# Optimization experiments

Hardware: AMD Instinct MI355X
Metric: run time of the kernel (lower is better)

## Reference

```python
import jax, jax.numpy as jnp
import numpy as np

B = 1_000_000
FEAT = 64
EMBEDDING_SIZE = 128


def setup_inputs() -> dict:
    key = jax.random.key(0)
    k0, k1, k2 = jax.random.split(key, 3)
    x = jax.random.normal(k0, (B, FEAT), dtype=jnp.float32)
    W1 = jax.random.normal(k1, (FEAT, FEAT), dtype=jnp.float32) * (1.0 / np.sqrt(FEAT))
    b1 = jnp.zeros((FEAT,), dtype=jnp.float32)
    W2 = jax.random.normal(k2, (FEAT, EMBEDDING_SIZE), dtype=jnp.float32) * (1.0 / np.sqrt(FEAT))
    b2 = jnp.zeros((EMBEDDING_SIZE,), dtype=jnp.float32)
    return {"x": x, "W1": W1, "b1": b1, "W2": W2, "b2": b2}


def reference(x, W1, b1, W2, b2):
    # head: Linear(64,64) -> ReLU -> Linear(64, EMBEDDING_SIZE)
    h = jax.nn.relu(x @ W1 + b1)
    e = h @ W2 + b2
    # per-sample L2 normalize with zero-norm guard (Normalize module)
    norm = jnp.linalg.norm(e, axis=-1, keepdims=True)  # [B,1]
    out = jnp.where(norm == 0, jnp.zeros_like(e), e / jnp.where(norm == 0, 1.0, norm))
    return out
```

## Files before the change

### kernel.cpp

```cpp
#include <hip/hip_runtime.h>
#include <stdint.h>


typedef __attribute__((ext_vector_type(8))) short short8;
typedef __attribute__((ext_vector_type(4))) float f32x4;

__device__ __forceinline__ ushort f2bf(float f) {
    union { float f; uint32_t u; } v; v.f = f;
    uint32_t u = v.u;
    u += 0x7fffu + ((u >> 16) & 1u);
    return (ushort)(u >> 16);
}

__global__ __launch_bounds__(256)
void fused_head_kernel(const float* __restrict__ x,
                       const float* __restrict__ W1,
                       const float* __restrict__ b1,
                       const float* __restrict__ W2,
                       const float* __restrict__ b2,
                       float* __restrict__ out,
                       int ntiles)
{
    __shared__ ushort w1t[64][72];
    __shared__ ushort w2t[128][72];
    __shared__ ushort htile[4][16][72];

    const int tid  = threadIdx.x;
    const int wave = tid >> 6;
    const int lane = tid & 63;
    const int l16  = lane & 15;
    const int lq   = lane >> 4;

    for (int idx = tid; idx < 64 * 64; idx += 256) {
        int k = idx >> 6, n = idx & 63;
        w1t[n][k] = f2bf(W1[idx]);
    }
    for (int idx = tid; idx < 64 * 128; idx += 256) {
        int k = idx >> 7, n = idx & 127;
        w2t[n][k] = f2bf(W2[idx]);
    }
    float b1v[4], b2v[8];
#pragma unroll
    for (int nt = 0; nt < 4; ++nt) b1v[nt] = b1[l16 + 16 * nt];
#pragma unroll
    for (int nt = 0; nt < 8; ++nt) b2v[nt] = b2[l16 + 16 * nt];
    __syncthreads();

    for (int tile = blockIdx.x; tile < ntiles; tile += gridDim.x) {
        const int r0 = tile * 64 + wave * 16;

        short8 xf[2];
#pragma unroll
        for (int t = 0; t < 2; ++t) {
            const float* p = x + (size_t)(r0 + l16) * 64 + t * 32 + lq * 8;
            f32x4 u0 = *(const f32x4*)p;
            f32x4 u1 = *(const f32x4*)(p + 4);
            short8 v;
            v[0] = (short)f2bf(u0[0]); v[1] = (short)f2bf(u0[1]);
            v[2] = (short)f2bf(u0[2]); v[3] = (short)f2bf(u0[3]);
            v[4] = (short)f2bf(u1[0]); v[5] = (short)f2bf(u1[1]);
            v[6] = (short)f2bf(u1[2]); v[7] = (short)f2bf(u1[3]);
            xf[t] = v;
        }

        f32x4 acc1[4] = {};
#pragma unroll
        for (int t = 0; t < 2; ++t) {
#pragma unroll
            for (int nt = 0; nt < 4; ++nt) {
                short8 bf = *(const short8*)&w1t[l16 + 16 * nt][t * 32 + lq * 8];
                acc1[nt] = __builtin_amdgcn_mfma_f32_16x16x32_bf16(xf[t], bf, acc1[nt], 0, 0, 0);
            }
        }
#pragma unroll
        for (int nt = 0; nt < 4; ++nt) {
#pragma unroll
            for (int r = 0; r < 4; ++r) {
                float h = acc1[nt][r] + b1v[nt];
                h = h > 0.f ? h : 0.f;
                htile[wave][lq * 4 + r][l16 + 16 * nt] = f2bf(h);
            }
        }

        f32x4 acc2[8] = {};
#pragma unroll
        for (int t = 0; t < 2; ++t) {
            short8 af = *(const short8*)&htile[wave][l16][t * 32 + lq * 8];
#pragma unroll
            for (int nt = 0; nt < 8; ++nt) {
                short8 bf = *(const short8*)&w2t[l16 + 16 * nt][t * 32 + lq * 8];
                acc2[nt] = __builtin_amdgcn_mfma_f32_16x16x32_bf16(af, bf, acc2[nt], 0, 0, 0);
            }
        }

        float ss[4] = {0.f, 0.f, 0.f, 0.f};
#pragma unroll
        for (int nt = 0; nt < 8; ++nt) {
#pragma unroll
            for (int r = 0; r < 4; ++r) {
                float e = acc2[nt][r] + b2v[nt];
                acc2[nt][r] = e;
                ss[r] += e * e;
            }
        }
#pragma unroll
        for (int m = 1; m < 16; m <<= 1) {
#pragma unroll
            for (int r = 0; r < 4; ++r) ss[r] += __shfl_xor(ss[r], m, 64);
        }

#pragma unroll
        for (int r = 0; r < 4; ++r) {
            float s = ss[r];
            float sc = s > 0.f ? rsqrtf(s) : 0.f;
            float* po = out + (size_t)(r0 + lq * 4 + r) * 128 + l16;
#pragma unroll
            for (int nt = 0; nt < 8; ++nt) po[nt * 16] = acc2[nt][r] * sc;
        }
    }
}

extern "C" void kernel_launch(void* const* d_in, const int* in_sizes, int n_in,
                              void* d_out, int out_size, void* d_ws, size_t ws_size,
                              hipStream_t stream) {
    const float* x  = (const float*)d_in[0];
    const float* W1 = (const float*)d_in[1];
    const float* b1 = (const float*)d_in[2];
    const float* W2 = (const float*)d_in[3];
    const float* b2 = (const float*)d_in[4];
    float* out = (float*)d_out;

    const int nrows  = in_sizes[0] / 64;
    const int ntiles = nrows / 64;
    int grid = ntiles < 3125 ? ntiles : 3125;

    hipLaunchKernelGGL(fused_head_kernel, dim3(grid), dim3(256), 0, stream,
                       x, W1, b1, W2, b2, out, ntiles);
}
```

Baseline: 676.5 us.

## Software-pipeline x loads, transpose MFMA operands for vectorized row-major stores

Double-buffers the per-tile x loads in registers, so the next tile's global reads are issued before the current tile is computed. The MFMA operand order is swapped so each lane holds four contiguous output columns of a single row. That allows 16-byte vector stores and a two-step shuffle reduction for the norm in place of a four-step one. Biases move to shared memory, read as float4, and launch bounds request 4 blocks per CU, which raises register pressure from the two prefetch buffers.

```diff
diff --git a/kernel.cpp b/kernel.cpp
--- a/kernel.cpp
+++ b/kernel.cpp
@@ -11,8 +11,11 @@
     u += 0x7fffu + ((u >> 16) & 1u);
     return (ushort)(u >> 16);
 }
+__device__ __forceinline__ uint32_t pack2(float a, float b) {
+    return (uint32_t)f2bf(a) | ((uint32_t)f2bf(b) << 16);
+}
 
-__global__ __launch_bounds__(256)
+__global__ __launch_bounds__(256, 4)
 void fused_head_kernel(const float* __restrict__ x,
                        const float* __restrict__ W1,
                        const float* __restrict__ b1,
@@ -24,12 +27,23 @@
     __shared__ ushort w1t[64][72];
     __shared__ ushort w2t[128][72];
     __shared__ ushort htile[4][16][72];
+    __shared__ __align__(16) float b1s[64];
+    __shared__ __align__(16) float b2s[128];
 
     const int tid  = threadIdx.x;
     const int wave = tid >> 6;
     const int lane = tid & 63;
     const int l16  = lane & 15;
     const int lq   = lane >> 4;
+
+    int tile = blockIdx.x;
+
+    f32x4 uA[4], uB[4];
+    {
+        const float* p = x + ((size_t)(tile * 64 + wave * 16 + l16)) * 64 + lq * 8;
+        uA[0] = *(const f32x4*)p;        uA[1] = *(const f32x4*)(p + 4);
+        uA[2] = *(const f32x4*)(p + 32); uA[3] = *(const f32x4*)(p + 36);
+    }
 
     for (int idx = tid; idx < 64 * 64; idx += 256) {
         int k = idx >> 6, n = idx & 63;
@@ -39,84 +53,97 @@
         int k = idx >> 7, n = idx & 127;
         w2t[n][k] = f2bf(W2[idx]);
     }
-    float b1v[4], b2v[8];
-#pragma unroll
-    for (int nt = 0; nt < 4; ++nt) b1v[nt] = b1[l16 + 16 * nt];
-#pragma unroll
-    for (int nt = 0; nt < 8; ++nt) b2v[nt] = b2[l16 + 16 * nt];
+    if (tid < 64)  b1s[tid] = b1[tid];
+    if (tid < 128) b2s[tid] = b2[tid];
     __syncthreads();
 
-    for (int tile = blockIdx.x; tile < ntiles; tile += gridDim.x) {
-        const int r0 = tile * 64 + wave * 16;
+    auto loadx = [&](f32x4* u, int t) {
+        const float* p = x + ((size_t)(t * 64 + wave * 16 + l16)) * 64 + lq * 8;
+        u[0] = *(const f32x4*)p;        u[1] = *(const f32x4*)(p + 4);
+        u[2] = *(const f32x4*)(p + 32); u[3] = *(const f32x4*)(p + 36);
+    };
 
+    auto process = [&](const f32x4* u, int t) {
         short8 xf[2];
 #pragma unroll
-        for (int t = 0; t < 2; ++t) {
-            const float* p = x + (size_t)(r0 + l16) * 64 + t * 32 + lq * 8;
-            f32x4 u0 = *(const f32x4*)p;
-            f32x4 u1 = *(const f32x4*)(p + 4);
+        for (int h = 0; h < 2; ++h) {
             short8 v;
-            v[0] = (short)f2bf(u0[0]); v[1] = (short)f2bf(u0[1]);
-            v[2] = (short)f2bf(u0[2]); v[3] = (short)f2bf(u0[3]);
-            v[4] = (short)f2bf(u1[0]); v[5] = (short)f2bf(u1[1]);
-            v[6] = (short)f2bf(u1[2]); v[7] = (short)f2bf(u1[3]);
-            xf[t] = v;
+            v[0] = (short)f2bf(u[2*h][0]);   v[1] = (short)f2bf(u[2*h][1]);
+            v[2] = (short)f2bf(u[2*h][2]);   v[3] = (short)f2bf(u[2*h][3]);
+            v[4] = (short)f2bf(u[2*h+1][0]); v[5] = (short)f2bf(u[2*h+1][1]);
+            v[6] = (short)f2bf(u[2*h+1][2]); v[7] = (short)f2bf(u[2*h+1][3]);
+            xf[h] = v;
         }
 
         f32x4 acc1[4] = {};
 #pragma unroll
-        for (int t = 0; t < 2; ++t) {
+        for (int h = 0; h < 2; ++h)
 #pragma unroll
             for (int nt = 0; nt < 4; ++nt) {
-                short8 bf = *(const short8*)&w1t[l16 + 16 * nt][t * 32 + lq * 8];
-                acc1[nt] = __builtin_amdgcn_mfma_f32_16x16x32_bf16(xf[t], bf, acc1[nt], 0, 0, 0);
+                short8 wf = *(const short8*)&w1t[nt * 16 + l16][h * 32 + lq * 8];
+                acc1[nt] = __builtin_amdgcn_mfma_f32_16x16x32_bf16(wf, xf[h], acc1[nt], 0, 0, 0);
             }
-        }
+
 #pragma unroll
         for (int nt = 0; nt < 4; ++nt) {
-#pragma unroll
-            for (int r = 0; r < 4; ++r) {
-                float h = acc1[nt][r] + b1v[nt];
-                h = h > 0.f ? h : 0.f;
-                htile[wave][lq * 4 + r][l16 + 16 * nt] = f2bf(h);
-            }
+            f32x4 bv = *(const f32x4*)&b1s[nt * 16 + lq * 4];
+            float h0 = acc1[nt][0] + bv[0]; h0 = h0 > 0.f ? h0 : 0.f;
+            float h1 = acc1[nt][1] + bv[1]; h1 = h1 > 0.f ? h1 : 0.f;
+            float h2 = acc1[nt][2] + bv[2]; h2 = h2 > 0.f ? h2 : 0.f;
+            float h3 = acc1[nt][3] + bv[3]; h3 = h3 > 0.f ? h3 : 0.f;
+            uint32_t* dst = (uint32_t*)&htile[wave][l16][nt * 16 + lq * 4];
+            dst[0] = pack2(h0, h1);
+            dst[1] = pack2(h2, h3);
         }
 
         f32x4 acc2[8] = {};
 #pragma unroll
-        for (int t = 0; t < 2; ++t) {
-            short8 af = *(const short8*)&htile[wave][l16][t * 32 + lq * 8];
+        for (int h = 0; h < 2; ++h) {
+            short8 hf = *(const short8*)&htile[wave][l16][h * 32 + lq * 8];
 #pragma unroll
             for (int nt = 0; nt < 8; ++nt) {
-                short8 bf = *(const short8*)&w2t[l16 + 16 * nt][t * 32 + lq * 8];
-                acc2[nt] = __builtin_amdgcn_mfma_f32_16x16x32_bf16(af, bf, acc2[nt], 0, 0, 0);
+                short8 wf = *(const short8*)&w2t[nt * 16 + l16][h * 32 + lq * 8];
+                acc2[nt] = __builtin_amdgcn_mfma_f32_16x16x32_bf16(wf, hf, acc2[nt], 0, 0, 0);
             }
         }
 
-        float ss[4] = {0.f, 0.f, 0.f, 0.f};
+        float ss = 0.f;
 #pragma unroll
         for (int nt = 0; nt < 8; ++nt) {
+            f32x4 bv = *(const f32x4*)&b2s[nt * 16 + lq * 4];
 #pragma unroll
             for (int r = 0; r < 4; ++r) {
-                float e = acc2[nt][r] + b2v[nt];
+                float e = acc2[nt][r] + bv[r];
                 acc2[nt][r] = e;
-                ss[r] += e * e;
+                ss += e * e;
             }
         }
+        ss += __shfl_xor(ss, 16, 64);
+        ss += __shfl_xor(ss, 32, 64);
+        float sc = ss > 0.f ? rsqrtf(ss) : 0.f;
+
+        float* po = out + ((size_t)(t * 64 + wave * 16 + l16)) * 128 + lq * 4;
 #pragma unroll
-        for (int m = 1; m < 16; m <<= 1) {
-#pragma unroll
-            for (int r = 0; r < 4; ++r) ss[r] += __shfl_xor(ss[r], m, 64);
+        for (int nt = 0; nt < 8; ++nt) {
+            f32x4 v;
+            v[0] = acc2[nt][0] * sc; v[1] = acc2[nt][1] * sc;
+            v[2] = acc2[nt][2] * sc; v[3] = acc2[nt][3] * sc;
+            *(f32x4*)(po + nt * 16) = v;
         }
+    };
 
-#pragma unroll
-        for (int r = 0; r < 4; ++r) {
-            float s = ss[r];
-            float sc = s > 0.f ? rsqrtf(s) : 0.f;
-            float* po = out + (size_t)(r0 + lq * 4 + r) * 128 + l16;
-#pragma unroll
-            for (int nt = 0; nt < 8; ++nt) po[nt * 16] = acc2[nt][r] * sc;
-        }
+    int next = tile + gridDim.x;
+    while (true) {
+        bool hasB = next < ntiles;
+        if (hasB) loadx(uB, next);
+        process(uA, tile);
+        if (!hasB) break;
+        tile = next; next += gridDim.x;
+        bool hasA = next < ntiles;
+        if (hasA) loadx(uA, next);
+        process(uB, tile);
+        if (!hasA) break;
+        tile = next; next += gridDim.x;
     }
 }
 
```

New measurement: 974.5 us. +44.0%, slower.
